# Kernel tuning notes

Hardware: AMD Instinct MI355X
Metric: run time of the kernel (lower is better)

Reference implementation:

```python
import jax, jax.numpy as jnp
import numpy as np

N_NODES, N_EDGES, D_FEAT, D_HID, K_CHEB = 30000, 480000, 256, 256, 2


def setup_inputs() -> dict:
    N, E, D, H, K = N_NODES, N_EDGES, D_FEAT, D_HID, K_CHEB
    key = jax.random.key(0)
    ks = jax.random.split(key, 24)
    sD = 1.0 / np.sqrt(D)
    sH = 1.0 / np.sqrt(H)
    inp = {
        "x": jax.random.normal(ks[0], (N, D), jnp.float32),
        "edge_index": jax.random.randint(ks[1], (2, E), 0, N),
        "edge_weight": jax.random.uniform(ks[2], (E,), jnp.float32),
        "h": jax.random.normal(ks[3], (N, H), jnp.float32),
        "c": jax.random.normal(ks[4], (N, H), jnp.float32),
        "src_neighbor_ids": jax.random.randint(ks[5], (E,), 0, N),
        "dst_neighbor_ids": jax.random.randint(ks[6], (E,), 0, N),
    }
    for j, nm in enumerate(["W_i", "W_f", "W_g", "W_o"]):
        inp[nm] = jax.random.normal(ks[7 + j], (D, H), jnp.float32) * sD
    for j, nm in enumerate(["Wc_i", "Wc_f", "Wc_g", "Wc_o"]):
        inp[nm] = jax.random.normal(ks[11 + j], (K, H, H), jnp.float32) * sH
    for nm in ["bc_i", "bc_f", "bc_g", "bc_o", "b_i", "b_f", "b_g", "b_o", "b_lin"]:
        inp[nm] = jnp.zeros((H,), jnp.float32)
    for j, nm in enumerate(["w_ci", "w_cf", "w_co"]):
        inp[nm] = jax.random.normal(ks[15 + j], (H,), jnp.float32) * 0.1
    inp["W_lin"] = jax.random.normal(ks[18], (H, H), jnp.float32) * sH
    return inp


def _cheb_conv(h, src, dst, norm, W, b):
    # ChebConv, K=2, sym norm, lambda_max=2: T0 = h, T1 = L_hat h = -D^-1/2 A D^-1/2 h
    out = h @ W[0]
    t1 = jax.ops.segment_sum(norm[:, None] * h[src], dst, num_segments=h.shape[0])
    return out + t1 @ W[1] + b


def reference(x, edge_index, edge_weight, h, c, src_neighbor_ids, dst_neighbor_ids,
              W_i, W_f, W_g, W_o, Wc_i, Wc_f, Wc_g, Wc_o,
              bc_i, bc_f, bc_g, bc_o, w_ci, w_cf, w_co,
              b_i, b_f, b_g, b_o, W_lin, b_lin):
    src, dst = edge_index[0], edge_index[1]
    n = x.shape[0]
    # neighbor-feature augmentation: gather both BEFORE any update, then scatter-add
    snf = x[src_neighbor_ids]
    dnf = x[dst_neighbor_ids]
    x = x.at[src].add(snf)
    x = x.at[dst].add(dnf)
    # symmetric Chebyshev normalization (lambda_max = 2 -> diagonal of L_hat is 0)
    deg = jax.ops.segment_sum(edge_weight, src, num_segments=n)
    dinv = jnp.where(deg > 0, jax.lax.rsqrt(jnp.maximum(deg, 1e-12)), 0.0)
    norm = -dinv[src] * edge_weight * dinv[dst]
    # GCLSTM gates
    i = jax.nn.sigmoid(x @ W_i + _cheb_conv(h, src, dst, norm, Wc_i, bc_i) + w_ci * c + b_i)
    f = jax.nn.sigmoid(x @ W_f + _cheb_conv(h, src, dst, norm, Wc_f, bc_f) + w_cf * c + b_f)
    g = jnp.tanh(x @ W_g + _cheb_conv(h, src, dst, norm, Wc_g, bc_g) + b_g)
    c_new = f * c + i * g
    o = jax.nn.sigmoid(x @ W_o + _cheb_conv(h, src, dst, norm, Wc_o, bc_o) + w_co * c_new + b_o)
    h0 = o * jnp.tanh(c_new)
    h_out = jax.nn.relu(h0) @ W_lin + b_lin
    return (h_out, h0, c_new)
```

## Files before the change

kernel.cpp:

```cpp
#include <hip/hip_runtime.h>
#include <math.h>

#define NN 30000
#define NE 480000
#define DH 256
#define NH (NN * DH)
#define MPAD 30080
#define CAP 64

typedef _Float16 f16x4 __attribute__((ext_vector_type(4)));
typedef _Float16 f16x8 __attribute__((ext_vector_type(8)));
typedef float f32x4 __attribute__((ext_vector_type(4)));

static __device__ __forceinline__ float sigmoidf_(float x) {
    return 1.0f / (1.0f + __expf(-x));
}

static __device__ __forceinline__ void gload16(const _Float16* g, _Float16* l) {
    __builtin_amdgcn_global_load_lds(
        (const __attribute__((address_space(1))) void*)g,
        (__attribute__((address_space(3))) void*)l, 16, 0, 0);
}


__global__ void deg_kernel(const int* __restrict__ src, const float* __restrict__ w,
                           float* __restrict__ deg) {
    int e = blockIdx.x * blockDim.x + threadIdx.x;
    if (e < NE) atomicAdd(&deg[src[e]], w[e]);
}

__global__ void dinv_kernel(float* __restrict__ deg) {
    int v = blockIdx.x * blockDim.x + threadIdx.x;
    if (v < NN) {
        float d = deg[v];
        deg[v] = (d > 0.0f) ? rsqrtf(fmaxf(d, 1e-12f)) : 0.0f;
    }
}

__global__ void scatter2(const int* __restrict__ src, const int* __restrict__ dst,
                         const int* __restrict__ snf, const int* __restrict__ dnf,
                         const float* __restrict__ w, const float* __restrict__ dinv,
                         int* __restrict__ cntS, int* __restrict__ cntD,
                         int* __restrict__ slotS, int2* __restrict__ slotD) {
    int e = blockIdx.x * blockDim.x + threadIdx.x;
    if (e >= NE) return;
    int s = src[e], d = dst[e];
    int pS = atomicAdd(&cntS[s], 1);
    if (pS < CAP) slotS[s * CAP + pS] = snf[e];
    float nrm = -dinv[s] * w[e] * dinv[d];
    int pD = atomicAdd(&cntD[d], 1);
    if (pD < CAP) slotD[d * CAP + pD] = make_int2(s | (dnf[e] << 15), __float_as_int(nrm));
}


__global__ void conv_f16(const float* __restrict__ in, _Float16* __restrict__ out, int n8) {
    int i = blockIdx.x * blockDim.x + threadIdx.x;
    if (i >= n8) return;
    const float4 a = *reinterpret_cast<const float4*>(&in[(size_t)i * 8]);
    const float4 b = *reinterpret_cast<const float4*>(&in[(size_t)i * 8 + 4]);
    f16x8 v;
    v[0] = (_Float16)a.x; v[1] = (_Float16)a.y; v[2] = (_Float16)a.z; v[3] = (_Float16)a.w;
    v[4] = (_Float16)b.x; v[5] = (_Float16)b.y; v[6] = (_Float16)b.z; v[7] = (_Float16)b.w;
    *reinterpret_cast<f16x8*>(&out[(size_t)i * 8]) = v;
}

__global__ __launch_bounds__(256) void fused_gather(const _Float16* __restrict__ x16,
                                                    const _Float16* __restrict__ h16,
                                                    const int* __restrict__ cntS,
                                                    const int* __restrict__ cntD,
                                                    const int4* __restrict__ slotS4,
                                                    const int4* __restrict__ slotD4,
                                                    _Float16* __restrict__ A16) {
    int wid = (blockIdx.x * blockDim.x + threadIdx.x) >> 6;
    int l = threadIdx.x & 63;
    if (wid >= NN) return;
    int nS = min(cntS[wid], CAP);
    int nD = min(cntD[wid], CAP);

    f16x4 xv = *reinterpret_cast<const f16x4*>(&x16[(size_t)wid * 256 + l * 4]);
    float a0 = (float)xv[0], a1 = (float)xv[1], a2 = (float)xv[2], a3 = (float)xv[3];
    float t0 = 0.f, t1 = 0.f, t2 = 0.f, t3 = 0.f;

    const int4* pS = &slotS4[(size_t)wid * (CAP / 4)];
    for (int j = 0; j < nS; j += 4) {
        int4 e = pS[j >> 2];
        f16x4 v0, v1, v2, v3;
        v0 = *reinterpret_cast<const f16x4*>(&x16[(size_t)e.x * 256 + l * 4]);
        if (j + 1 < nS) v1 = *reinterpret_cast<const f16x4*>(&x16[(size_t)e.y * 256 + l * 4]);
        if (j + 2 < nS) v2 = *reinterpret_cast<const f16x4*>(&x16[(size_t)e.z * 256 + l * 4]);
        if (j + 3 < nS) v3 = *reinterpret_cast<const f16x4*>(&x16[(size_t)e.w * 256 + l * 4]);
        a0 += (float)v0[0]; a1 += (float)v0[1]; a2 += (float)v0[2]; a3 += (float)v0[3];
        if (j + 1 < nS) { a0 += (float)v1[0]; a1 += (float)v1[1]; a2 += (float)v1[2]; a3 += (float)v1[3]; }
        if (j + 2 < nS) { a0 += (float)v2[0]; a1 += (float)v2[1]; a2 += (float)v2[2]; a3 += (float)v2[3]; }
        if (j + 3 < nS) { a0 += (float)v3[0]; a1 += (float)v3[1]; a2 += (float)v3[2]; a3 += (float)v3[3]; }
    }

    const int4* pD = &slotD4[(size_t)wid * (CAP / 2)];
    for (int j = 0; j < nD; j += 4) {
        int4 ea = pD[(j >> 2) * 2];
        int4 eb = pD[(j >> 2) * 2 + 1];
        int p0 = ea.x, p1 = ea.z, p2 = eb.x, p3 = eb.z;
        float n0 = __int_as_float(ea.y), n1f = __int_as_float(ea.w);
        float n2f = __int_as_float(eb.y), n3f = __int_as_float(eb.w);
        f16x4 x0, x1, x2, x3, g0, g1, g2, g3;
        x0 = *reinterpret_cast<const f16x4*>(&x16[(size_t)(p0 >> 15) * 256 + l * 4]);
        g0 = *reinterpret_cast<const f16x4*>(&h16[(size_t)(p0 & 0x7fff) * 256 + l * 4]);
        if (j + 1 < nD) {
            x1 = *reinterpret_cast<const f16x4*>(&x16[(size_t)(p1 >> 15) * 256 + l * 4]);
            g1 = *reinterpret_cast<const f16x4*>(&h16[(size_t)(p1 & 0x7fff) * 256 + l * 4]);
        }
        if (j + 2 < nD) {
            x2 = *reinterpret_cast<const f16x4*>(&x16[(size_t)(p2 >> 15) * 256 + l * 4]);
            g2 = *reinterpret_cast<const f16x4*>(&h16[(size_t)(p2 & 0x7fff) * 256 + l * 4]);
        }
        if (j + 3 < nD) {
            x3 = *reinterpret_cast<const f16x4*>(&x16[(size_t)(p3 >> 15) * 256 + l * 4]);
            g3 = *reinterpret_cast<const f16x4*>(&h16[(size_t)(p3 & 0x7fff) * 256 + l * 4]);
        }
        a0 += (float)x0[0]; a1 += (float)x0[1]; a2 += (float)x0[2]; a3 += (float)x0[3];
        t0 += n0 * (float)g0[0]; t1 += n0 * (float)g0[1];
        t2 += n0 * (float)g0[2]; t3 += n0 * (float)g0[3];
        if (j + 1 < nD) {
            a0 += (float)x1[0]; a1 += (float)x1[1]; a2 += (float)x1[2]; a3 += (float)x1[3];
            t0 += n1f * (float)g1[0]; t1 += n1f * (float)g1[1];
            t2 += n1f * (float)g1[2]; t3 += n1f * (float)g1[3];
        }
        if (j + 2 < nD) {
            a0 += (float)x2[0]; a1 += (float)x2[1]; a2 += (float)x2[2]; a3 += (float)x2[3];
            t0 += n2f * (float)g2[0]; t1 += n2f * (float)g2[1];
            t2 += n2f * (float)g2[2]; t3 += n2f * (float)g2[3];
        }
        if (j + 3 < nD) {
            a0 += (float)x3[0]; a1 += (float)x3[1]; a2 += (float)x3[2]; a3 += (float)x3[3];
            t0 += n3f * (float)g3[0]; t1 += n3f * (float)g3[1];
            t2 += n3f * (float)g3[2]; t3 += n3f * (float)g3[3];
        }
    }

    f16x4 hrow = *reinterpret_cast<const f16x4*>(&h16[(size_t)wid * 256 + l * 4]);
    f16x4 oX, oT;
    oX[0] = (_Float16)a0; oX[1] = (_Float16)a1; oX[2] = (_Float16)a2; oX[3] = (_Float16)a3;
    oT[0] = (_Float16)t0; oT[1] = (_Float16)t1; oT[2] = (_Float16)t2; oT[3] = (_Float16)t3;
    size_t rb = (size_t)wid * 768;
    *reinterpret_cast<f16x4*>(&A16[rb + l * 4]) = oX;
    *reinterpret_cast<f16x4*>(&A16[rb + 256 + l * 4]) = hrow;
    *reinterpret_cast<f16x4*>(&A16[rb + 512 + l * 4]) = oT;
}


__global__ void wcatT_kernel(const float* __restrict__ W_i, const float* __restrict__ W_f,
                             const float* __restrict__ W_g, const float* __restrict__ W_o,
                             const float* __restrict__ Wc_i, const float* __restrict__ Wc_f,
                             const float* __restrict__ Wc_g, const float* __restrict__ Wc_o,
                             _Float16* __restrict__ WcatT) {
    int idx = blockIdx.x * blockDim.x + threadIdx.x;
    if (idx >= 768 * 1024) return;
    int k = idx >> 10, n = idx & 1023;
    int seg = k >> 8, kk = k & 255, gate = n >> 8, nn = n & 255;
    const float* p;
    if (seg == 0) {
        p = (gate == 0) ? W_i : (gate == 1) ? W_f : (gate == 2) ? W_g : W_o;
    } else {
        const float* base = (gate == 0) ? Wc_i : (gate == 1) ? Wc_f : (gate == 2) ? Wc_g : Wc_o;
        p = base + (seg - 1) * 65536;
    }
    WcatT[(size_t)n * 768 + k] = (_Float16)p[kk * 256 + nn];
}

__global__ void wlinT_kernel(const float* __restrict__ W_lin, _Float16* __restrict__ WlinT) {
    int idx = blockIdx.x * blockDim.x + threadIdx.x;
    if (idx >= 256 * 256) return;
    int k = idx >> 8, n = idx & 255;
    WlinT[(size_t)n * 256 + k] = (_Float16)W_lin[k * 256 + n];
}


template <int K, int N, bool HALF_OUT>
__global__ __launch_bounds__(256) void gemm16(const _Float16* __restrict__ A,
                                              const _Float16* __restrict__ B,
                                              const float* __restrict__ bias,
                                              _Float16* __restrict__ outH,
                                              float* __restrict__ outF) {
    __shared__ _Float16 As[128 * 64];
    __shared__ _Float16 Bs[128 * 64];
    int tid = threadIdx.x;
    int w = tid >> 6, l = tid & 63;
    int wy = w >> 1, wx = w & 1;
    int bm = blockIdx.x * 128, bn = blockIdx.y * 128;

    f32x4 acc[4][4];
    #pragma unroll
    for (int m = 0; m < 4; ++m)
        #pragma unroll
        for (int n = 0; n < 4; ++n)
            acc[m][n] = (f32x4){0.f, 0.f, 0.f, 0.f};

    int rowi = tid >> 3;
    int g = (tid & 7) ^ (rowi & 7);
    const _Float16* gA0 = A + (size_t)(bm + rowi) * K + g * 8;
    const _Float16* gB0 = B + (size_t)(bn + rowi) * K + g * 8;

    for (int kt = 0; kt < K; kt += 64) {
        #pragma unroll
        for (int i = 0; i < 4; ++i) {
            gload16(gA0 + kt + (size_t)i * 32 * K, &As[i * 2048 + w * 512]);
            gload16(gB0 + kt + (size_t)i * 32 * K, &Bs[i * 2048 + w * 512]);
        }
        __syncthreads();

        f16x8 af[4][2], bf[4][2];
        #pragma unroll
        for (int m = 0; m < 4; ++m) {
            int row = wy * 64 + m * 16 + (l & 15);
            #pragma unroll
            for (int ks = 0; ks < 2; ++ks) {
                int ch = (ks * 4 + (l >> 4)) ^ (l & 7);
                af[m][ks] = *reinterpret_cast<const f16x8*>(&As[row * 64 + ch * 8]);
            }
        }
        #pragma unroll
        for (int n = 0; n < 4; ++n) {
            int row = wx * 64 + n * 16 + (l & 15);
            #pragma unroll
            for (int ks = 0; ks < 2; ++ks) {
                int ch = (ks * 4 + (l >> 4)) ^ (l & 7);
                bf[n][ks] = *reinterpret_cast<const f16x8*>(&Bs[row * 64 + ch * 8]);
            }
        }
        #pragma unroll
        for (int ks = 0; ks < 2; ++ks)
            #pragma unroll
            for (int m = 0; m < 4; ++m)
                #pragma unroll
                for (int n = 0; n < 4; ++n)
                    acc[m][n] = __builtin_amdgcn_mfma_f32_16x16x32_f16(
                        af[m][ks], bf[n][ks], acc[m][n], 0, 0, 0);
        __syncthreads();
    }

    #pragma unroll
    for (int m = 0; m < 4; ++m) {
        #pragma unroll
        for (int n = 0; n < 4; ++n) {
            int col = bn + wx * 64 + n * 16 + (l & 15);
            #pragma unroll
            for (int j = 0; j < 4; ++j) {
                int row = bm + wy * 64 + m * 16 + (l >> 4) * 4 + j;
                if (row < NN) {
                    if constexpr (HALF_OUT)
                        outH[(size_t)row * N + col] = (_Float16)acc[m][n][j];
                    else
                        outF[(size_t)row * N + col] = acc[m][n][j] + bias[col];
                }
            }
        }
    }
}


__global__ void gate_kernel(const _Float16* __restrict__ pre, const float* __restrict__ c,
                            const float* __restrict__ bc_i, const float* __restrict__ bc_f,
                            const float* __restrict__ bc_g, const float* __restrict__ bc_o,
                            const float* __restrict__ b_i, const float* __restrict__ b_f,
                            const float* __restrict__ b_g, const float* __restrict__ b_o,
                            const float* __restrict__ w_ci, const float* __restrict__ w_cf,
                            const float* __restrict__ w_co,
                            float* __restrict__ h0p, float* __restrict__ cnp,
                            _Float16* __restrict__ relu16) {
    int idx = blockIdx.x * blockDim.x + threadIdx.x;
    if (idx >= NN * 64) return;
    int row = idx >> 6;
    int n4 = (idx & 63) << 2;
    size_t pb = (size_t)row * 1024;
    f16x4 pi = *reinterpret_cast<const f16x4*>(&pre[pb + n4]);
    f16x4 pf = *reinterpret_cast<const f16x4*>(&pre[pb + 256 + n4]);
    f16x4 pg = *reinterpret_cast<const f16x4*>(&pre[pb + 512 + n4]);
    f16x4 po = *reinterpret_cast<const f16x4*>(&pre[pb + 768 + n4]);
    float4 cv = *reinterpret_cast<const float4*>(&c[(size_t)row * 256 + n4]);
    float4 vbci = *reinterpret_cast<const float4*>(&bc_i[n4]);
    float4 vbcf = *reinterpret_cast<const float4*>(&bc_f[n4]);
    float4 vbcg = *reinterpret_cast<const float4*>(&bc_g[n4]);
    float4 vbco = *reinterpret_cast<const float4*>(&bc_o[n4]);
    float4 vbi  = *reinterpret_cast<const float4*>(&b_i[n4]);
    float4 vbf  = *reinterpret_cast<const float4*>(&b_f[n4]);
    float4 vbg  = *reinterpret_cast<const float4*>(&b_g[n4]);
    float4 vbo  = *reinterpret_cast<const float4*>(&b_o[n4]);
    float4 vwci = *reinterpret_cast<const float4*>(&w_ci[n4]);
    float4 vwcf = *reinterpret_cast<const float4*>(&w_cf[n4]);
    float4 vwco = *reinterpret_cast<const float4*>(&w_co[n4]);
    const float* CV = (const float*)&cv;
    const float* BCI = (const float*)&vbci; const float* BCF = (const float*)&vbcf;
    const float* BCG = (const float*)&vbcg; const float* BCO = (const float*)&vbco;
    const float* BI = (const float*)&vbi;   const float* BF = (const float*)&vbf;
    const float* BG = (const float*)&vbg;   const float* BO = (const float*)&vbo;
    const float* WCI = (const float*)&vwci; const float* WCF = (const float*)&vwcf;
    const float* WCO = (const float*)&vwco;
    float4 cn4, h04;
    float* CN = (float*)&cn4; float* H0 = (float*)&h04;
    f16x4 rl;
    #pragma unroll
    for (int j = 0; j < 4; ++j) {
        float iv = sigmoidf_((float)pi[j] + BCI[j] + BI[j] + WCI[j] * CV[j]);
        float fv = sigmoidf_((float)pf[j] + BCF[j] + BF[j] + WCF[j] * CV[j]);
        float gv = tanhf((float)pg[j] + BCG[j] + BG[j]);
        float cn = fv * CV[j] + iv * gv;
        float ov = sigmoidf_((float)po[j] + BCO[j] + BO[j] + WCO[j] * cn);
        CN[j] = cn;
        float h0 = ov * tanhf(cn);
        H0[j] = h0;
        rl[j] = (_Float16)fmaxf(h0, 0.f);
    }
    *reinterpret_cast<float4*>(&cnp[(size_t)row * 256 + n4]) = cn4;
    *reinterpret_cast<float4*>(&h0p[(size_t)row * 256 + n4]) = h04;
    *reinterpret_cast<f16x4*>(&relu16[(size_t)row * 256 + n4]) = rl;
}


extern "C" void kernel_launch(void* const* d_in, const int* in_sizes, int n_in,
                              void* d_out, int out_size, void* d_ws, size_t ws_size,
                              hipStream_t stream) {
    const float* x   = (const float*)d_in[0];
    const int*   ei  = (const int*)d_in[1];
    const float* ew  = (const float*)d_in[2];
    const float* h   = (const float*)d_in[3];
    const float* c   = (const float*)d_in[4];
    const int*   snf = (const int*)d_in[5];
    const int*   dnf = (const int*)d_in[6];
    const float* W_i = (const float*)d_in[7];
    const float* W_f = (const float*)d_in[8];
    const float* W_g = (const float*)d_in[9];
    const float* W_o = (const float*)d_in[10];
    const float* Wc_i = (const float*)d_in[11];
    const float* Wc_f = (const float*)d_in[12];
    const float* Wc_g = (const float*)d_in[13];
    const float* Wc_o = (const float*)d_in[14];
    const float* bc_i = (const float*)d_in[15];
    const float* bc_f = (const float*)d_in[16];
    const float* bc_g = (const float*)d_in[17];
    const float* bc_o = (const float*)d_in[18];
    const float* b_i  = (const float*)d_in[19];
    const float* b_f  = (const float*)d_in[20];
    const float* b_g  = (const float*)d_in[21];
    const float* b_o  = (const float*)d_in[22];
    const float* b_lin = (const float*)d_in[23];
    const float* w_ci = (const float*)d_in[24];
    const float* w_cf = (const float*)d_in[25];
    const float* w_co = (const float*)d_in[26];
    const float* W_lin = (const float*)d_in[27];

    const int* src = ei;
    const int* dst = ei + NE;

    float* out = (float*)d_out;
    float* houtp = out;
    float* h0p   = out + NH;
    float* cnp   = out + 2 * NH;

    char* ws = (char*)d_ws;
    _Float16* pre16 = (_Float16*)ws;
    int* cntS = (int*)ws;
    int* cntD = (int*)(ws + 131072);
    int* slotS = (int*)(ws + 262144);
    int2* slotD = (int2*)(ws + 7942144);
    _Float16* h16 = (_Float16*)(ws + 23302144);

    _Float16* A16 = (_Float16*)(ws + 61440000);
    _Float16* A16lin = A16;
    _Float16* WcatT = (_Float16*)(ws + 107642880);
    _Float16* WlinT = (_Float16*)(ws + 109215744);
    float* deg = (float*)(ws + 109346816);
    _Float16* x16 = (_Float16*)(ws + 109477888);

    hipMemsetAsync(deg, 0, 131072, stream);
    hipMemsetAsync(cntS, 0, 262144, stream);

    deg_kernel<<<(NE + 255) / 256, 256, 0, stream>>>(src, ew, deg);
    dinv_kernel<<<(NN + 255) / 256, 256, 0, stream>>>(deg);

    conv_f16<<<3750, 256, 0, stream>>>(x, x16, NN * 32);
    conv_f16<<<3750, 256, 0, stream>>>(h, h16, NN * 32);

    scatter2<<<(NE + 255) / 256, 256, 0, stream>>>(src, dst, snf, dnf, ew, deg,
                                                   cntS, cntD, slotS, slotD);

    fused_gather<<<7500, 256, 0, stream>>>(x16, h16, cntS, cntD,
                                           (const int4*)slotS, (const int4*)slotD, A16);
    hipMemsetAsync((char*)A16 + (size_t)NN * 768 * 2, 0, (size_t)(MPAD - NN) * 768 * 2, stream);

    wcatT_kernel<<<3072, 256, 0, stream>>>(W_i, W_f, W_g, W_o, Wc_i, Wc_f, Wc_g, Wc_o, WcatT);
    wlinT_kernel<<<256, 256, 0, stream>>>(W_lin, WlinT);

    dim3 g1(MPAD / 128, 1024 / 128);
    gemm16<768, 1024, true><<<g1, 256, 0, stream>>>(A16, WcatT, nullptr, pre16, nullptr);

    gate_kernel<<<7500, 256, 0, stream>>>(pre16, c, bc_i, bc_f, bc_g, bc_o,
                                          b_i, b_f, b_g, b_o, w_ci, w_cf, w_co,
                                          h0p, cnp, A16lin);
    hipMemsetAsync((char*)A16lin + (size_t)NN * 256 * 2, 0, (size_t)(MPAD - NN) * 256 * 2, stream);

    dim3 g2(MPAD / 128, 256 / 128);
    gemm16<256, 256, false><<<g2, 256, 0, stream>>>(A16lin, WlinT, b_lin, nullptr, houtp);
}
```

Before: 364.3 us.

## Merge prep kernels, fold pad-zeroing into kernels, swizzle gate GEMM tiles

Measured after the change: 337.0 us. 7.5% less time.

```diff
diff --git a/kernel.cpp b/kernel.cpp
--- a/kernel.cpp
+++ b/kernel.cpp
@@ -23,10 +23,28 @@
 }
 
 
-__global__ void deg_kernel(const int* __restrict__ src, const float* __restrict__ w,
-                           float* __restrict__ deg) {
-    int e = blockIdx.x * blockDim.x + threadIdx.x;
-    if (e < NE) atomicAdd(&deg[src[e]], w[e]);
+__global__ void prep0(const int* __restrict__ src, const float* __restrict__ ew,
+                      float* __restrict__ deg,
+                      const float* __restrict__ x, _Float16* __restrict__ x16,
+                      const float* __restrict__ h, _Float16* __restrict__ h16) {
+    int b = blockIdx.x;
+    if (b < 1875) {
+        int e = b * 256 + threadIdx.x;
+        if (e < NE) atomicAdd(&deg[src[e]], ew[e]);
+        return;
+    }
+    int i = (b - 1875) * 256 + threadIdx.x;
+    const int n8 = NN * 32;
+    const float* in; _Float16* out; int idx;
+    if (i < n8) { in = x; out = x16; idx = i; }
+    else if (i < 2 * n8) { in = h; out = h16; idx = i - n8; }
+    else return;
+    const float4 p = *reinterpret_cast<const float4*>(&in[(size_t)idx * 8]);
+    const float4 q = *reinterpret_cast<const float4*>(&in[(size_t)idx * 8 + 4]);
+    f16x8 v;
+    v[0] = (_Float16)p.x; v[1] = (_Float16)p.y; v[2] = (_Float16)p.z; v[3] = (_Float16)p.w;
+    v[4] = (_Float16)q.x; v[5] = (_Float16)q.y; v[6] = (_Float16)q.z; v[7] = (_Float16)q.w;
+    *reinterpret_cast<f16x8*>(&out[(size_t)idx * 8]) = v;
 }
 
 __global__ void dinv_kernel(float* __restrict__ deg) {
@@ -52,18 +70,6 @@
     if (pD < CAP) slotD[d * CAP + pD] = make_int2(s | (dnf[e] << 15), __float_as_int(nrm));
 }
 
-
-__global__ void conv_f16(const float* __restrict__ in, _Float16* __restrict__ out, int n8) {
-    int i = blockIdx.x * blockDim.x + threadIdx.x;
-    if (i >= n8) return;
-    const float4 a = *reinterpret_cast<const float4*>(&in[(size_t)i * 8]);
-    const float4 b = *reinterpret_cast<const float4*>(&in[(size_t)i * 8 + 4]);
-    f16x8 v;
-    v[0] = (_Float16)a.x; v[1] = (_Float16)a.y; v[2] = (_Float16)a.z; v[3] = (_Float16)a.w;
-    v[4] = (_Float16)b.x; v[5] = (_Float16)b.y; v[6] = (_Float16)b.z; v[7] = (_Float16)b.w;
-    *reinterpret_cast<f16x8*>(&out[(size_t)i * 8]) = v;
-}
-
 __global__ __launch_bounds__(256) void fused_gather(const _Float16* __restrict__ x16,
                                                     const _Float16* __restrict__ h16,
                                                     const int* __restrict__ cntS,
@@ -73,11 +79,20 @@
                                                     _Float16* __restrict__ A16) {
     int wid = (blockIdx.x * blockDim.x + threadIdx.x) >> 6;
     int l = threadIdx.x & 63;
-    if (wid >= NN) return;
+    if (wid >= MPAD) return;
+    size_t rb = (size_t)wid * 768;
+    if (wid >= NN) {
+        f16x4 z = {};
+        *reinterpret_cast<f16x4*>(&A16[rb + l * 4]) = z;
+        *reinterpret_cast<f16x4*>(&A16[rb + 256 + l * 4]) = z;
+        *reinterpret_cast<f16x4*>(&A16[rb + 512 + l * 4]) = z;
+        return;
+    }
     int nS = min(cntS[wid], CAP);
     int nD = min(cntD[wid], CAP);
 
     f16x4 xv = *reinterpret_cast<const f16x4*>(&x16[(size_t)wid * 256 + l * 4]);
+    f16x4 hrow = *reinterpret_cast<const f16x4*>(&h16[(size_t)wid * 256 + l * 4]);
     float a0 = (float)xv[0], a1 = (float)xv[1], a2 = (float)xv[2], a3 = (float)xv[3];
     float t0 = 0.f, t1 = 0.f, t2 = 0.f, t3 = 0.f;
 
@@ -137,45 +152,43 @@
         }
     }
 
-    f16x4 hrow = *reinterpret_cast<const f16x4*>(&h16[(size_t)wid * 256 + l * 4]);
     f16x4 oX, oT;
     oX[0] = (_Float16)a0; oX[1] = (_Float16)a1; oX[2] = (_Float16)a2; oX[3] = (_Float16)a3;
     oT[0] = (_Float16)t0; oT[1] = (_Float16)t1; oT[2] = (_Float16)t2; oT[3] = (_Float16)t3;
-    size_t rb = (size_t)wid * 768;
     *reinterpret_cast<f16x4*>(&A16[rb + l * 4]) = oX;
     *reinterpret_cast<f16x4*>(&A16[rb + 256 + l * 4]) = hrow;
     *reinterpret_cast<f16x4*>(&A16[rb + 512 + l * 4]) = oT;
 }
 
 
-__global__ void wcatT_kernel(const float* __restrict__ W_i, const float* __restrict__ W_f,
+__global__ void wpack_kernel(const float* __restrict__ W_i, const float* __restrict__ W_f,
                              const float* __restrict__ W_g, const float* __restrict__ W_o,
                              const float* __restrict__ Wc_i, const float* __restrict__ Wc_f,
                              const float* __restrict__ Wc_g, const float* __restrict__ Wc_o,
-                             _Float16* __restrict__ WcatT) {
+                             const float* __restrict__ W_lin,
+                             _Float16* __restrict__ WcatT, _Float16* __restrict__ WlinT) {
     int idx = blockIdx.x * blockDim.x + threadIdx.x;
-    if (idx >= 768 * 1024) return;
-    int k = idx >> 10, n = idx & 1023;
-    int seg = k >> 8, kk = k & 255, gate = n >> 8, nn = n & 255;
-    const float* p;
-    if (seg == 0) {
-        p = (gate == 0) ? W_i : (gate == 1) ? W_f : (gate == 2) ? W_g : W_o;
+    if (idx < 768 * 1024) {
+        int k = idx >> 10, n = idx & 1023;
+        int seg = k >> 8, kk = k & 255, gate = n >> 8, nn = n & 255;
+        const float* p;
+        if (seg == 0) {
+            p = (gate == 0) ? W_i : (gate == 1) ? W_f : (gate == 2) ? W_g : W_o;
+        } else {
+            const float* base = (gate == 0) ? Wc_i : (gate == 1) ? Wc_f : (gate == 2) ? Wc_g : Wc_o;
+            p = base + (seg - 1) * 65536;
+        }
+        WcatT[(size_t)n * 768 + k] = (_Float16)p[kk * 256 + nn];
     } else {
-        const float* base = (gate == 0) ? Wc_i : (gate == 1) ? Wc_f : (gate == 2) ? Wc_g : Wc_o;
-        p = base + (seg - 1) * 65536;
-    }
-    WcatT[(size_t)n * 768 + k] = (_Float16)p[kk * 256 + nn];
-}
-
-__global__ void wlinT_kernel(const float* __restrict__ W_lin, _Float16* __restrict__ WlinT) {
-    int idx = blockIdx.x * blockDim.x + threadIdx.x;
-    if (idx >= 256 * 256) return;
-    int k = idx >> 8, n = idx & 255;
-    WlinT[(size_t)n * 256 + k] = (_Float16)W_lin[k * 256 + n];
-}
-
-
-template <int K, int N, bool HALF_OUT>
+        int i2 = idx - 768 * 1024;
+        if (i2 >= 256 * 256) return;
+        int k = i2 >> 8, n = i2 & 255;
+        WlinT[(size_t)n * 256 + k] = (_Float16)W_lin[k * 256 + n];
+    }
+}
+
+
+template <int K, int N, bool HALF_OUT, bool SWZ1D>
 __global__ __launch_bounds__(256) void gemm16(const _Float16* __restrict__ A,
                                               const _Float16* __restrict__ B,
                                               const float* __restrict__ bias,
@@ -186,7 +199,17 @@
     int tid = threadIdx.x;
     int w = tid >> 6, l = tid & 63;
     int wy = w >> 1, wx = w & 1;
-    int bm = blockIdx.x * 128, bn = blockIdx.y * 128;
+    int bm, bn;
+    if constexpr (SWZ1D) {
+        constexpr int NT = N / 128;
+        constexpr int TOT = (MPAD / 128) * NT;
+        constexpr int CH = TOT / 8;
+        int b = blockIdx.x;
+        int v = (b & 7) * CH + (b >> 3);
+        bm = (v / NT) * 128; bn = (v % NT) * 128;
+    } else {
+        bm = blockIdx.x * 128; bn = blockIdx.y * 128;
+    }
 
     f32x4 acc[4][4];
     #pragma unroll
@@ -268,9 +291,14 @@
                             float* __restrict__ h0p, float* __restrict__ cnp,
                             _Float16* __restrict__ relu16) {
     int idx = blockIdx.x * blockDim.x + threadIdx.x;
-    if (idx >= NN * 64) return;
+    if (idx >= MPAD * 64) return;
     int row = idx >> 6;
     int n4 = (idx & 63) << 2;
+    if (row >= NN) {
+        f16x4 z = {};
+        *reinterpret_cast<f16x4*>(&relu16[(size_t)row * 256 + n4]) = z;
+        return;
+    }
     size_t pb = (size_t)row * 1024;
     f16x4 pi = *reinterpret_cast<const f16x4*>(&pre[pb + n4]);
     f16x4 pf = *reinterpret_cast<const f16x4*>(&pre[pb + 256 + n4]);
@@ -360,44 +388,37 @@
     _Float16* pre16 = (_Float16*)ws;
     int* cntS = (int*)ws;
     int* cntD = (int*)(ws + 131072);
-    int* slotS = (int*)(ws + 262144);
-    int2* slotD = (int2*)(ws + 7942144);
-    _Float16* h16 = (_Float16*)(ws + 23302144);
+    float* deg = (float*)(ws + 262144);
+    int* slotS = (int*)(ws + 393216);
+    int2* slotD = (int2*)(ws + 8073216);
+    _Float16* h16 = (_Float16*)(ws + 23433216);
 
     _Float16* A16 = (_Float16*)(ws + 61440000);
     _Float16* A16lin = A16;
     _Float16* WcatT = (_Float16*)(ws + 107642880);
     _Float16* WlinT = (_Float16*)(ws + 109215744);
-    float* deg = (float*)(ws + 109346816);
-    _Float16* x16 = (_Float16*)(ws + 109477888);
-
-    hipMemsetAsync(deg, 0, 131072, stream);
-    hipMemsetAsync(cntS, 0, 262144, stream);
-
-    deg_kernel<<<(NE + 255) / 256, 256, 0, stream>>>(src, ew, deg);
-    dinv_kernel<<<(NN + 255) / 256, 256, 0, stream>>>(deg);
-
-    conv_f16<<<3750, 256, 0, stream>>>(x, x16, NN * 32);
-    conv_f16<<<3750, 256, 0, stream>>>(h, h16, NN * 32);
-
-    scatter2<<<(NE + 255) / 256, 256, 0, stream>>>(src, dst, snf, dnf, ew, deg,
-                                                   cntS, cntD, slotS, slotD);
-
-    fused_gather<<<7500, 256, 0, stream>>>(x16, h16, cntS, cntD,
+    _Float16* x16 = (_Float16*)(ws + 109346816);
+
+    hipMemsetAsync(ws, 0, 393216, stream);
+
+    prep0<<<9375, 256, 0, stream>>>(src, ew, deg, x, x16, h, h16);
+    dinv_kernel<<<118, 256, 0, stream>>>(deg);
+
+    scatter2<<<1875, 256, 0, stream>>>(src, dst, snf, dnf, ew, deg,
+                                       cntS, cntD, slotS, slotD);
+
+    fused_gather<<<7520, 256, 0, stream>>>(x16, h16, cntS, cntD,
                                            (const int4*)slotS, (const int4*)slotD, A16);
-    hipMemsetAsync((char*)A16 + (size_t)NN * 768 * 2, 0, (size_t)(MPAD - NN) * 768 * 2, stream);
-
-    wcatT_kernel<<<3072, 256, 0, stream>>>(W_i, W_f, W_g, W_o, Wc_i, Wc_f, Wc_g, Wc_o, WcatT);
-    wlinT_kernel<<<256, 256, 0, stream>>>(W_lin, WlinT);
-
-    dim3 g1(MPAD / 128, 1024 / 128);
-    gemm16<768, 1024, true><<<g1, 256, 0, stream>>>(A16, WcatT, nullptr, pre16, nullptr);
-
-    gate_kernel<<<7500, 256, 0, stream>>>(pre16, c, bc_i, bc_f, bc_g, bc_o,
+
+    wpack_kernel<<<3328, 256, 0, stream>>>(W_i, W_f, W_g, W_o, Wc_i, Wc_f, Wc_g, Wc_o,
+                                           W_lin, WcatT, WlinT);
+
+    gemm16<768, 1024, true, true><<<1880, 256, 0, stream>>>(A16, WcatT, nullptr, pre16, nullptr);
+
+    gate_kernel<<<7520, 256, 0, stream>>>(pre16, c, bc_i, bc_f, bc_g, bc_o,
                                           b_i, b_f, b_g, b_o, w_ci, w_cf, w_co,
                                           h0p, cnp, A16lin);
-    hipMemsetAsync((char*)A16lin + (size_t)NN * 256 * 2, 0, (size_t)(MPAD - NN) * 256 * 2, stream);
 
     dim3 g2(MPAD / 128, 256 / 128);
-    gemm16<256, 256, false><<<g2, 256, 0, stream>>>(A16lin, WlinT, b_lin, nullptr, houtp);
-}
+    gemm16<256, 256, false, false><<<g2, 256, 0, stream>>>(A16lin, WlinT, b_lin, nullptr, houtp);
+}
```
